# Kernel optimization log

Measured on AMD Instinct MI355X. Metric: run time of the kernel, lower is better.

Reference implementation:

```python
import jax, jax.numpy as jnp
import numpy as np

# RoIAlign config (matches init_kwargs)
OUT_H, OUT_W = 7, 7
SPATIAL_SCALE = 0.25
SAMPLE_NUM = 2  # sampling points per bin side (static)


def setup_inputs() -> dict:
    key = jax.random.key(0)
    k0, k1, k2, k3 = jax.random.split(key, 4)
    B, C, H, W = 2, 256, 200, 336
    N = 1024
    img_h, img_w = H / SPATIAL_SCALE, W / SPATIAL_SCALE
    features = jax.random.normal(k0, (B, C, H, W), dtype=jnp.float32)
    # build valid rois: [batch_idx, x1, y1, x2, y2] in image coordinates
    bidx = jax.random.randint(k1, (N,), 0, B).astype(jnp.float32)
    ctr = jax.random.uniform(k2, (N, 2)) * jnp.array([img_w, img_h], jnp.float32)
    wh = (0.05 + 0.35 * jax.random.uniform(k3, (N, 2))) * jnp.array([img_w, img_h], jnp.float32)
    x1y1 = jnp.clip(ctr - wh / 2, 0.0)
    x2y2 = jnp.minimum(ctr + wh / 2, jnp.array([img_w, img_h], jnp.float32))
    rois = jnp.concatenate([bidx[:, None], x1y1[:, 0:1], x1y1[:, 1:2], x2y2[:, 0:1], x2y2[:, 1:2]], axis=1)
    return {"features": features, "rois": rois}


def _roi_align(features, rois):
    B, C, H, W = features.shape
    N = rois.shape[0]
    ns = SAMPLE_NUM
    P, Q = OUT_H * ns, OUT_W * ns  # full sampling grid per roi

    bidx = rois[:, 0].astype(jnp.int32)
    x1 = rois[:, 1] * SPATIAL_SCALE
    y1 = rois[:, 2] * SPATIAL_SCALE
    x2 = rois[:, 3] * SPATIAL_SCALE
    y2 = rois[:, 4] * SPATIAL_SCALE
    roi_w = jnp.maximum(x2 - x1, 1.0)  # aligned=False legacy semantics
    roi_h = jnp.maximum(y2 - y1, 1.0)
    bin_w = roi_w / OUT_W
    bin_h = roi_h / OUT_H

    # sample coords: y = y1 + (p + 0.5) * bin_h / ns, p in [0, P)
    ys = y1[:, None] + (jnp.arange(P, dtype=jnp.float32) + 0.5) * (bin_h[:, None] / ns)  # (N,P)
    xs = x1[:, None] + (jnp.arange(Q, dtype=jnp.float32) + 0.5) * (bin_w[:, None] / ns)  # (N,Q)

    # out-of-bound samples contribute zero (kernel skips y<-1 or y>H)
    ymask = (ys >= -1.0) & (ys <= H)
    xmask = (xs >= -1.0) & (xs <= W)
    y = jnp.clip(ys, 0.0, H - 1)
    x = jnp.clip(xs, 0.0, W - 1)
    y0 = jnp.floor(y).astype(jnp.int32)
    x0 = jnp.floor(x).astype(jnp.int32)
    y1i = jnp.minimum(y0 + 1, H - 1)
    x1i = jnp.minimum(x0 + 1, W - 1)
    ly = y - y0.astype(jnp.float32)
    lx = x - x0.astype(jnp.float32)
    hy, hx = 1.0 - ly, 1.0 - lx

    b = bidx[:, None, None]            # (N,1,1)
    def gather(yi, xi):                # -> (N,P,Q,C)
        return features[b, :, yi[:, :, None], xi[:, None, :]]
    f00 = gather(y0, x0)
    f01 = gather(y0, x1i)
    f10 = gather(y1i, x0)
    f11 = gather(y1i, x1i)

    wy0, wy1 = hy[:, :, None, None], ly[:, :, None, None]  # (N,P,1,1)
    wx0, wx1 = hx[:, None, :, None], lx[:, None, :, None]  # (N,1,Q,1)
    val = wy0 * (wx0 * f00 + wx1 * f01) + wy1 * (wx0 * f10 + wx1 * f11)
    val = val * (ymask[:, :, None, None] & xmask[:, None, :, None])

    # average the ns x ns samples per output bin
    val = val.reshape(N, OUT_H, ns, OUT_W, ns, C).mean(axis=(2, 4))  # (N,OUT_H,OUT_W,C)
    return jnp.transpose(val, (0, 3, 1, 2))  # (N,C,OUT_H,OUT_W)


def reference(features, rois):
    return _roi_align(features, rois)
```

## Files before the change

### kernel.cpp

```cpp
#include <hip/hip_runtime.h>
#include <hip/hip_fp16.h>

#define BB   2
#define CCH  256
#define HH   200
#define WW   336
#define HWN  (HH * WW)
#define OH   7
#define OW   7
#define SCALEF 0.25f
#define NBIN (OH * OW)
#define PER_ROI (CCH * NBIN)
#define NBANDS 8
#define NBUCK (BB * NBANDS)
#define CHALF 128
#define HALF_OUT (CHALF * NBIN)

typedef float  nfloat4 __attribute__((ext_vector_type(4)));
typedef unsigned short ushort8v __attribute__((ext_vector_type(8)));

__device__ __forceinline__ __half2 u32_as_h2(unsigned int u) {
    union { unsigned int u; __half2 h; } c;
    c.u = u;
    return c.h;
}

__global__ __launch_bounds__(256) void transpose_f16_k(const float* __restrict__ src,
                                                       unsigned short* __restrict__ dst,
                                                       const float* __restrict__ rois,
                                                       int N, int* __restrict__ perm) {
    __shared__ unsigned short t16[64 * 128];
    __shared__ int cnt[NBUCK], off[NBUCK];
    __shared__ unsigned char keys[1024];

    const int tx  = threadIdx.x;
    const int ty  = threadIdx.y;
    const int tid = ty * 16 + tx;

    if (blockIdx.x == 0 && blockIdx.y == 0 && blockIdx.z == 0) {
        if (N > 1024 || N < 8) {
            for (int i = tid; i < N; i += 256) perm[i] = i;
        } else {
            if (tid < NBUCK) cnt[tid] = 0;
            __syncthreads();
            for (int i = tid; i < N; i += 256) {
                const float* r = rois + i * 5;
                const int b = (int)r[0];
                const float yc = (r[2] + r[4]) * 0.5f * SCALEF;
                int band = (int)(yc * ((float)NBANDS / (float)HH));
                band = min(max(band, 0), NBANDS - 1);
                const int k = b * NBANDS + band;
                keys[i] = (unsigned char)k;
                atomicAdd(&cnt[k], 1);
            }
            __syncthreads();
            if (tid == 0) {
                int s = 0;
                for (int k = 0; k < NBUCK; ++k) { off[k] = s; s += cnt[k]; }
            }
            __syncthreads();
            for (int i = tid; i < N; i += 256) {
                perm[atomicAdd(&off[keys[i]], 1)] = i;
            }
        }
        __syncthreads();
    }

    const int b   = blockIdx.z;
    const int hw0 = blockIdx.x * 64;
    const int c0  = blockIdx.y * 128;

#pragma unroll
    for (int r = 0; r < 8; ++r) {
        const int cl = ty + r * 16;
        const nfloat4 v = __builtin_nontemporal_load(
            (const nfloat4*)(src + (size_t)(b * CCH + c0 + cl) * HWN + hw0 + tx * 4));
        const int cz = (((cl >> 3) ^ tx) << 3) + (cl & 7);
        t16[(tx * 4 + 0) * 128 + cz] = __half_as_ushort(__float2half(v.x));
        t16[(tx * 4 + 1) * 128 + cz] = __half_as_ushort(__float2half(v.y));
        t16[(tx * 4 + 2) * 128 + cz] = __half_as_ushort(__float2half(v.z));
        t16[(tx * 4 + 3) * 128 + cz] = __half_as_ushort(__float2half(v.w));
    }
    __syncthreads();

    const int cg = tid & 15;
#pragma unroll
    for (int wv = 0; wv < 4; ++wv) {
        const int hwl = (tid >> 4) + wv * 16;
        const ushort8v o = *(const ushort8v*)&t16[hwl * 128 + ((cg ^ (hwl >> 2)) << 3)];
        *(ushort8v*)(dst + (size_t)(b * HWN + hw0 + hwl) * CCH + c0 + cg * 8) = o;
    }
}

__global__ __launch_bounds__(512, 8) void roi_align_f16_k(const unsigned short* __restrict__ f,
                                                          const float* __restrict__ rois,
                                                          const int* __restrict__ perm,
                                                          float* __restrict__ out) {
    const int nblk = gridDim.x;
    int p;
    if ((nblk & 7) == 0) {
        p = (blockIdx.x & 7) * (nblk >> 3) + (blockIdx.x >> 3);
    } else {
        p = blockIdx.x;
    }
    const int n    = perm[p];
    const int cb   = blockIdx.y;
    const int tid  = threadIdx.x;
    const int lane = tid & 63;
    const int l16  = lane & 15;
    const int qx   = (lane >> 4) & 1;
    const int qy   = lane >> 5;
    const int g    = tid >> 6;
    const int c8   = l16 * 8;

    __shared__ __align__(16) float buf_f[HALF_OUT];
    __shared__ int   s_yb[2][14];
    __shared__ int   s_xb[2][14];
    __shared__ float s_wy[2][14];
    __shared__ float s_wx[2][14];

    const float* r = rois + n * 5;
    const int   b   = (int)r[0];
    const float rx1 = r[1] * SCALEF, ry1 = r[2] * SCALEF;
    const float rx2 = r[3] * SCALEF, ry2 = r[4] * SCALEF;
    const float bw = fmaxf(rx2 - rx1, 1.0f) * (1.0f / OW);
    const float bh = fmaxf(ry2 - ry1, 1.0f) * (1.0f / OH);

    if (tid < 14) {
        const float ys = ry1 + ((float)tid + 0.5f) * (bh * 0.5f);
        const float vy = (ys >= -1.0f && ys <= (float)HH) ? 0.5f : 0.0f;
        const float y = fminf(fmaxf(ys, 0.0f), (float)(HH - 1));
        const int y0  = (int)floorf(y);
        const int y1  = min(y0 + 1, HH - 1);
        const float ly = y - (float)y0;
        s_yb[0][tid] = (b * HH + y0) * (WW * CCH);
        s_yb[1][tid] = (b * HH + y1) * (WW * CCH);
        s_wy[0][tid] = (1.0f - ly) * vy;
        s_wy[1][tid] = ly * vy;
    } else if (tid >= 64 && tid < 78) {
        const int j = tid - 64;
        const float xs = rx1 + ((float)j + 0.5f) * (bw * 0.5f);
        const float vx = (xs >= -1.0f && xs <= (float)WW) ? 0.5f : 0.0f;
        const float x = fminf(fmaxf(xs, 0.0f), (float)(WW - 1));
        const int x0  = (int)floorf(x);
        const int x1  = min(x0 + 1, WW - 1);
        const float lx = x - (float)x0;
        s_xb[0][j] = x0 * CCH;
        s_xb[1][j] = x1 * CCH;
        s_wx[0][j] = (1.0f - lx) * vx;
        s_wx[1][j] = lx * vx;
    }
    __syncthreads();

    const unsigned short* fp = f + cb * CHALF + c8;

    for (int bin = g; bin < NBIN; bin += 8) {
        const int ph = bin / OW;
        const int pw = bin - ph * OW;
        float acc[8] = {0.f, 0.f, 0.f, 0.f, 0.f, 0.f, 0.f, 0.f};
#pragma unroll
        for (int iy = 0; iy < 2; ++iy) {
            const int py   = ph * 2 + iy;
            const int ybs  = s_yb[qy][py];
            const float wy = s_wy[qy][py];
#pragma unroll
            for (int ix = 0; ix < 2; ++ix) {
                const int px  = pw * 2 + ix;
                const float w = wy * s_wx[qx][px];
                const uint4 q = *(const uint4*)(fp + ybs + s_xb[qx][px]);
                const float2 f0 = __half22float2(u32_as_h2(q.x));
                const float2 f1 = __half22float2(u32_as_h2(q.y));
                const float2 f2 = __half22float2(u32_as_h2(q.z));
                const float2 f3 = __half22float2(u32_as_h2(q.w));
                acc[0] += w * f0.x;  acc[1] += w * f0.y;
                acc[2] += w * f1.x;  acc[3] += w * f1.y;
                acc[4] += w * f2.x;  acc[5] += w * f2.y;
                acc[6] += w * f3.x;  acc[7] += w * f3.y;
            }
        }
#pragma unroll
        for (int j = 0; j < 8; ++j) {
            acc[j] += __shfl_xor(acc[j], 16);
            acc[j] += __shfl_xor(acc[j], 32);
        }
        if (lane < 16) {
#pragma unroll
            for (int j = 0; j < 8; ++j) {
                buf_f[(c8 + j) * NBIN + bin] = acc[j];
            }
        }
    }
    __syncthreads();

    nfloat4* ob = (nfloat4*)(out + (size_t)n * PER_ROI + cb * HALF_OUT);
    const nfloat4* bb = (const nfloat4*)buf_f;
    for (int i = tid; i < HALF_OUT / 4; i += 512) {
        __builtin_nontemporal_store(bb[i], ob + i);
    }
}

__global__ __launch_bounds__(256) void roi_align_direct_k(const float* __restrict__ f,
                                                          const float* __restrict__ rois,
                                                          float* __restrict__ out) {
    const int n   = blockIdx.x;
    const int c   = threadIdx.x;

    __shared__ int   s_y0[14], s_y1[14], s_x0[14], s_x1[14];
    __shared__ float s_ly[14], s_lx[14], s_vy[14], s_vx[14];

    const float* r = rois + n * 5;
    const int   b   = (int)r[0];
    const float rx1 = r[1] * SCALEF, ry1 = r[2] * SCALEF;
    const float rx2 = r[3] * SCALEF, ry2 = r[4] * SCALEF;
    const float bw = fmaxf(rx2 - rx1, 1.0f) * (1.0f / OW);
    const float bh = fmaxf(ry2 - ry1, 1.0f) * (1.0f / OH);

    if (c < 14) {
        const float ys = ry1 + ((float)c + 0.5f) * (bh * 0.5f);
        s_vy[c] = (ys >= -1.0f && ys <= (float)HH) ? 1.0f : 0.0f;
        const float y = fminf(fmaxf(ys, 0.0f), (float)(HH - 1));
        const int y0  = (int)floorf(y);
        s_y0[c] = y0 * WW;
        s_y1[c] = min(y0 + 1, HH - 1) * WW;
        s_ly[c] = y - (float)y0;
    } else if (c >= 64 && c < 78) {
        const int j = c - 64;
        const float xs = rx1 + ((float)j + 0.5f) * (bw * 0.5f);
        s_vx[j] = (xs >= -1.0f && xs <= (float)WW) ? 1.0f : 0.0f;
        const float x = fminf(fmaxf(xs, 0.0f), (float)(WW - 1));
        const int x0  = (int)floorf(x);
        s_x0[j] = x0;
        s_x1[j] = min(x0 + 1, WW - 1);
        s_lx[j] = x - (float)x0;
    }
    __syncthreads();

    const float* fb = f + (size_t)(b * CCH + c) * HWN;
    for (int bin = 0; bin < NBIN; ++bin) {
        const int ph = bin / OW, pw = bin - ph * OW;
        float acc = 0.0f;
        for (int iy = 0; iy < 2; ++iy) {
            const int py = ph * 2 + iy;
            const float ly = s_ly[py], hy = 1.0f - ly;
            for (int ix = 0; ix < 2; ++ix) {
                const int px = pw * 2 + ix;
                const float lx = s_lx[px], hx = 1.0f - lx;
                const float m = s_vy[py] * s_vx[px] * 0.25f;
                acc += m * (hy * (hx * fb[s_y0[py] + s_x0[px]] + lx * fb[s_y0[py] + s_x1[px]]) +
                            ly * (hx * fb[s_y1[py] + s_x0[px]] + lx * fb[s_y1[py] + s_x1[px]]));
            }
        }
        out[(size_t)n * PER_ROI + c * NBIN + bin] = acc;
    }
}

extern "C" void kernel_launch(void* const* d_in, const int* in_sizes, int n_in,
                              void* d_out, int out_size, void* d_ws, size_t ws_size,
                              hipStream_t stream) {
    const float* feat = (const float*)d_in[0];
    const float* rois = (const float*)d_in[1];
    float* out = (float*)d_out;
    const int N = in_sizes[1] / 5;

    const size_t tensor_bytes = (size_t)BB * CCH * HWN * sizeof(unsigned short);
    const size_t need = tensor_bytes + (size_t)N * sizeof(int);
    if (ws_size >= need) {
        unsigned short* fcl = (unsigned short*)d_ws;
        int* perm = (int*)((char*)d_ws + tensor_bytes);
        transpose_f16_k<<<dim3(HWN / 64, CCH / 128, BB), dim3(16, 16), 0, stream>>>(
            feat, fcl, rois, N, perm);
        roi_align_f16_k<<<dim3(N, 2), 512, 0, stream>>>(fcl, rois, perm, out);
    } else {
        roi_align_direct_k<<<N, 256, 0, stream>>>(feat, rois, out);
    }
}
```

Measured before the change: 235.2 us.

## Process full channel range per ROI block with per-lane channels and fp16 staging

Each block now handles all 256 channels of one ROI instead of splitting channels across two blocks. Every lane owns 4 channels and loads all four bilinear corners itself, which removes the cross-lane shuffle reduction and the shared-memory coordinate tables. Bin results are staged in shared memory as fp16 to halve LDS usage, then widened to fp32 on store. The grid is half as large, each lane issues narrower 8-byte loads, and the extra fp16 rounding of the outputs costs some accuracy.

```diff
diff --git a/kernel.cpp b/kernel.cpp
--- a/kernel.cpp
+++ b/kernel.cpp
@@ -13,8 +13,6 @@
 #define PER_ROI (CCH * NBIN)
 #define NBANDS 8
 #define NBUCK (BB * NBANDS)
-#define CHALF 128
-#define HALF_OUT (CHALF * NBIN)
 
 typedef float  nfloat4 __attribute__((ext_vector_type(4)));
 typedef unsigned short ushort8v __attribute__((ext_vector_type(8)));
@@ -103,99 +101,96 @@
     } else {
         p = blockIdx.x;
     }
-    const int n    = perm[p];
-    const int cb   = blockIdx.y;
-    const int tid  = threadIdx.x;
-    const int lane = tid & 63;
-    const int l16  = lane & 15;
-    const int qx   = (lane >> 4) & 1;
-    const int qy   = lane >> 5;
-    const int g    = tid >> 6;
-    const int c8   = l16 * 8;
-
-    __shared__ __align__(16) float buf_f[HALF_OUT];
-    __shared__ int   s_yb[2][14];
-    __shared__ int   s_xb[2][14];
-    __shared__ float s_wy[2][14];
-    __shared__ float s_wx[2][14];
+    const int n   = perm[p];
+    const int tid = threadIdx.x;
+    const int wv  = tid >> 6;
+    const int c4  = (tid & 63) * 4;
+
+    __shared__ __align__(16) unsigned short buf_h[PER_ROI];
 
     const float* r = rois + n * 5;
     const int   b   = (int)r[0];
     const float rx1 = r[1] * SCALEF, ry1 = r[2] * SCALEF;
     const float rx2 = r[3] * SCALEF, ry2 = r[4] * SCALEF;
-    const float bw = fmaxf(rx2 - rx1, 1.0f) * (1.0f / OW);
-    const float bh = fmaxf(ry2 - ry1, 1.0f) * (1.0f / OH);
-
-    if (tid < 14) {
-        const float ys = ry1 + ((float)tid + 0.5f) * (bh * 0.5f);
-        const float vy = (ys >= -1.0f && ys <= (float)HH) ? 0.5f : 0.0f;
-        const float y = fminf(fmaxf(ys, 0.0f), (float)(HH - 1));
-        const int y0  = (int)floorf(y);
-        const int y1  = min(y0 + 1, HH - 1);
-        const float ly = y - (float)y0;
-        s_yb[0][tid] = (b * HH + y0) * (WW * CCH);
-        s_yb[1][tid] = (b * HH + y1) * (WW * CCH);
-        s_wy[0][tid] = (1.0f - ly) * vy;
-        s_wy[1][tid] = ly * vy;
-    } else if (tid >= 64 && tid < 78) {
-        const int j = tid - 64;
-        const float xs = rx1 + ((float)j + 0.5f) * (bw * 0.5f);
-        const float vx = (xs >= -1.0f && xs <= (float)WW) ? 0.5f : 0.0f;
-        const float x = fminf(fmaxf(xs, 0.0f), (float)(WW - 1));
-        const int x0  = (int)floorf(x);
-        const int x1  = min(x0 + 1, WW - 1);
-        const float lx = x - (float)x0;
-        s_xb[0][j] = x0 * CCH;
-        s_xb[1][j] = x1 * CCH;
-        s_wx[0][j] = (1.0f - lx) * vx;
-        s_wx[1][j] = lx * vx;
-    }
-    __syncthreads();
-
-    const unsigned short* fp = f + cb * CHALF + c8;
-
-    for (int bin = g; bin < NBIN; bin += 8) {
+    const float bw2 = fmaxf(rx2 - rx1, 1.0f) * (0.5f / OW);
+    const float bh2 = fmaxf(ry2 - ry1, 1.0f) * (0.5f / OH);
+
+    const unsigned short* fp = f + (size_t)b * HH * WW * CCH + c4;
+
+    for (int bin = wv; bin < NBIN; bin += 8) {
         const int ph = bin / OW;
         const int pw = bin - ph * OW;
-        float acc[8] = {0.f, 0.f, 0.f, 0.f, 0.f, 0.f, 0.f, 0.f};
+
+        float wy[2][2], wx[2][2];
+        int   rb[2][2], cb[2][2];
 #pragma unroll
         for (int iy = 0; iy < 2; ++iy) {
-            const int py   = ph * 2 + iy;
-            const int ybs  = s_yb[qy][py];
-            const float wy = s_wy[qy][py];
-#pragma unroll
-            for (int ix = 0; ix < 2; ++ix) {
-                const int px  = pw * 2 + ix;
-                const float w = wy * s_wx[qx][px];
-                const uint4 q = *(const uint4*)(fp + ybs + s_xb[qx][px]);
-                const float2 f0 = __half22float2(u32_as_h2(q.x));
-                const float2 f1 = __half22float2(u32_as_h2(q.y));
-                const float2 f2 = __half22float2(u32_as_h2(q.z));
-                const float2 f3 = __half22float2(u32_as_h2(q.w));
-                acc[0] += w * f0.x;  acc[1] += w * f0.y;
-                acc[2] += w * f1.x;  acc[3] += w * f1.y;
-                acc[4] += w * f2.x;  acc[5] += w * f2.y;
-                acc[6] += w * f3.x;  acc[7] += w * f3.y;
-            }
-        }
-#pragma unroll
-        for (int j = 0; j < 8; ++j) {
-            acc[j] += __shfl_xor(acc[j], 16);
-            acc[j] += __shfl_xor(acc[j], 32);
-        }
-        if (lane < 16) {
-#pragma unroll
-            for (int j = 0; j < 8; ++j) {
-                buf_f[(c8 + j) * NBIN + bin] = acc[j];
-            }
-        }
+            const float ys = ry1 + ((float)(ph * 2 + iy) + 0.5f) * bh2;
+            const float vy = (ys >= -1.0f && ys <= (float)HH) ? 0.5f : 0.0f;
+            const float y  = fminf(fmaxf(ys, 0.0f), (float)(HH - 1));
+            const int y0   = (int)y;
+            const float ly = y - (float)y0;
+            rb[iy][0] = y0 * (WW * CCH);
+            rb[iy][1] = min(y0 + 1, HH - 1) * (WW * CCH);
+            wy[iy][0] = (1.0f - ly) * vy;
+            wy[iy][1] = ly * vy;
+        }
+#pragma unroll
+        for (int ix = 0; ix < 2; ++ix) {
+            const float xs = rx1 + ((float)(pw * 2 + ix) + 0.5f) * bw2;
+            const float vx = (xs >= -1.0f && xs <= (float)WW) ? 0.5f : 0.0f;
+            const float x  = fminf(fmaxf(xs, 0.0f), (float)(WW - 1));
+            const int x0   = (int)x;
+            const float lx = x - (float)x0;
+            cb[ix][0] = x0 * CCH;
+            cb[ix][1] = min(x0 + 1, WW - 1) * CCH;
+            wx[ix][0] = (1.0f - lx) * vx;
+            wx[ix][1] = lx * vx;
+        }
+
+        float a0 = 0.f, a1 = 0.f, a2 = 0.f, a3 = 0.f;
+#pragma unroll
+        for (int iy = 0; iy < 2; ++iy) {
+#pragma unroll
+            for (int ty = 0; ty < 2; ++ty) {
+                const int   rbase = rb[iy][ty];
+                const float wyy   = wy[iy][ty];
+#pragma unroll
+                for (int ix = 0; ix < 2; ++ix) {
+#pragma unroll
+                    for (int tx2 = 0; tx2 < 2; ++tx2) {
+                        const float w = wyy * wx[ix][tx2];
+                        const uint2 q = *(const uint2*)(fp + rbase + cb[ix][tx2]);
+                        const float2 f0 = __half22float2(u32_as_h2(q.x));
+                        const float2 f1 = __half22float2(u32_as_h2(q.y));
+                        a0 += w * f0.x;  a1 += w * f0.y;
+                        a2 += w * f1.x;  a3 += w * f1.y;
+                    }
+                }
+            }
+        }
+
+        const int sb = c4 * NBIN + bin;
+        buf_h[sb           ] = __half_as_ushort(__float2half(a0));
+        buf_h[sb +     NBIN] = __half_as_ushort(__float2half(a1));
+        buf_h[sb + 2 * NBIN] = __half_as_ushort(__float2half(a2));
+        buf_h[sb + 3 * NBIN] = __half_as_ushort(__float2half(a3));
     }
     __syncthreads();
 
-    nfloat4* ob = (nfloat4*)(out + (size_t)n * PER_ROI + cb * HALF_OUT);
-    const nfloat4* bb = (const nfloat4*)buf_f;
-    for (int i = tid; i < HALF_OUT / 4; i += 512) {
-        __builtin_nontemporal_store(bb[i], ob + i);
+    nfloat4* ob = (nfloat4*)(out + (size_t)n * PER_ROI);
+    const uint4* bb = (const uint4*)buf_h;
+    for (int i = tid; i < PER_ROI / 8; i += 512) {
+        const uint4 q = bb[i];
+        const __half2 h0 = u32_as_h2(q.x), h1 = u32_as_h2(q.y);
+        const __half2 h2 = u32_as_h2(q.z), h3 = u32_as_h2(q.w);
+        nfloat4 v0, v1;
+        v0.x = __low2float(h0);  v0.y = __high2float(h0);
+        v0.z = __low2float(h1);  v0.w = __high2float(h1);
+        v1.x = __low2float(h2);  v1.y = __high2float(h2);
+        v1.z = __low2float(h3);  v1.w = __high2float(h3);
+        __builtin_nontemporal_store(v0, ob + 2 * i);
+        __builtin_nontemporal_store(v1, ob + 2 * i + 1);
     }
 }
 
@@ -269,7 +264,7 @@
         int* perm = (int*)((char*)d_ws + tensor_bytes);
         transpose_f16_k<<<dim3(HWN / 64, CCH / 128, BB), dim3(16, 16), 0, stream>>>(
             feat, fcl, rois, N, perm);
-        roi_align_f16_k<<<dim3(N, 2), 512, 0, stream>>>(fcl, rois, perm, out);
+        roi_align_f16_k<<<dim3(N), 512, 0, stream>>>(fcl, rois, perm, out);
     } else {
         roi_align_direct_k<<<N, 256, 0, stream>>>(feat, rois, out);
     }
```

New measurement: 244.3 us. 3.9% more time.
